# Kernel optimization log

Measured on AMD Instinct MI355X. Metric: run time of the kernel, lower is better.

## Reference

```python
import jax, jax.numpy as jnp
import numpy as np

GROUPS = 32
EPS = 1e-5


def _group_norm(x, w, b):
    B, C, H, W = x.shape
    xr = x.reshape(B, GROUPS, C // GROUPS, H, W)
    mean = xr.mean(axis=(2, 3, 4), keepdims=True)
    var = xr.var(axis=(2, 3, 4), keepdims=True)
    xn = ((xr - mean) * jax.lax.rsqrt(var + EPS)).reshape(B, C, H, W)
    return xn * w[None, :, None, None] + b[None, :, None, None]


def _conv1x1(w, b, x):
    # 1x1 conv == per-pixel channel matmul
    return jnp.einsum('oc,bchw->bohw', w, x) + b[None, :, None, None]


def setup_inputs() -> dict:
    key = jax.random.key(0)
    ks = jax.random.split(key, 6)
    C = 512
    s = 1.0 / np.sqrt(C)  # kaiming-uniform-ish scale for 1x1 convs
    return {
        'x': jax.random.normal(ks[0], (4, C, 64, 64), jnp.float32),
        'gn_w': jnp.ones((C,), jnp.float32),
        'gn_b': jnp.zeros((C,), jnp.float32),
        'qw': jax.random.normal(ks[1], (C, C), jnp.float32) * s,
        'qb': jnp.zeros((C,), jnp.float32),
        'kw': jax.random.normal(ks[2], (C, C), jnp.float32) * s,
        'kb': jnp.zeros((C,), jnp.float32),
        'vw': jax.random.normal(ks[3], (C, C), jnp.float32) * s,
        'vb': jnp.zeros((C,), jnp.float32),
        'pw': jax.random.normal(ks[4], (C, C), jnp.float32) * s,
        'pb': jnp.zeros((C,), jnp.float32),
    }


def reference(x, gn_w, gn_b, qw, qb, kw, kb, vw, vb, pw, pb):
    B, C, H, W = x.shape
    h_ = _group_norm(x, gn_w, gn_b)
    q = _conv1x1(qw, qb, h_).reshape(B, C, H * W)
    k = _conv1x1(kw, kb, h_).reshape(B, C, H * W)
    v = _conv1x1(vw, vb, h_).reshape(B, C, H * W)
    # scores [B, HW(query), HW(key)]
    scores = jnp.einsum('bcq,bck->bqk', q, k) * (C ** -0.5)
    attn = jax.nn.softmax(scores, axis=-1)
    out = jnp.einsum('bqk,bdk->bdq', attn, v).reshape(B, C, H, W)
    return x + _conv1x1(pw, pb, out)
```

## Files before the change

### kernel.cpp

```cpp
#include <hip/hip_runtime.h>

#define DEV __device__ __forceinline__

typedef __attribute__((ext_vector_type(8))) short short8;
typedef __attribute__((ext_vector_type(4))) float floatx4;
typedef __attribute__((ext_vector_type(16))) float floatx16;
typedef __attribute__((ext_vector_type(4))) int i32x4;
typedef __attribute__((ext_vector_type(8))) int i32x8;

DEV unsigned short f2bs(float x) {
    unsigned u = __float_as_uint(x);
    unsigned r = (u + 0x7fffu + ((u >> 16) & 1u)) >> 16;
    return (unsigned short)r;
}

DEV unsigned char f2fp8(float x) {
#if __has_builtin(__builtin_amdgcn_cvt_pk_fp8_f32)
    int pk = __builtin_amdgcn_cvt_pk_fp8_f32(x, 0.f, 0, false);
    return (unsigned char)(pk & 0xff);
#else
    unsigned u = __float_as_uint(x);
    unsigned s = (u >> 24) & 0x80;
    unsigned a = u & 0x7fffffff;
    unsigned um = a + 0x7ffffu + ((a >> 20) & 1u);
    unsigned r = (a >= 0x3c800000u) ? ((um >> 20) - 0x3C0u) : 0u;
    return (unsigned char)(r | s);
#endif
}

DEV unsigned pack_fp8x4(float v0, float v1, float v2, float v3) {
#if __has_builtin(__builtin_amdgcn_cvt_pk_fp8_f32)
    unsigned pk = (unsigned)__builtin_amdgcn_cvt_pk_fp8_f32(v0, v1, 0, false);
    pk = (unsigned)__builtin_amdgcn_cvt_pk_fp8_f32(v2, v3, (int)pk, true);
    return pk;
#else
    return (unsigned)f2fp8(v0) | ((unsigned)f2fp8(v1) << 8) |
           ((unsigned)f2fp8(v2) << 16) | ((unsigned)f2fp8(v3) << 24);
#endif
}

DEV unsigned pack_i8x4(float v0, float v1, float v2, float v3) {
    unsigned b0 = (unsigned)((int)rintf(v0)) & 255u;
    unsigned b1 = (unsigned)((int)rintf(v1)) & 255u;
    unsigned b2 = (unsigned)((int)rintf(v2)) & 255u;
    unsigned b3 = (unsigned)((int)rintf(v3)) & 255u;
    return b0 | (b1 << 8) | (b2 << 16) | (b3 << 24);
}

DEV void syncfull() {
    asm volatile("s_waitcnt vmcnt(0) lgkmcnt(0)" ::: "memory");
    __builtin_amdgcn_sched_barrier(0);
    __builtin_amdgcn_s_barrier();
    __builtin_amdgcn_sched_barrier(0);
}

__global__ void pre_kernel(const float* __restrict__ x,
                           const float* __restrict__ qw, const float* __restrict__ kw,
                           const float* __restrict__ vw, const float* __restrict__ pw,
                           const float* __restrict__ qb, const float* __restrict__ kb,
                           unsigned short* __restrict__ wqkb, unsigned short* __restrict__ wvb,
                           unsigned short* __restrict__ wpb,
                           float* __restrict__ biasqk,
                           float* __restrict__ stats) {
    int b = blockIdx.x, tid = threadIdx.x;
    if (b < 768) {
        const float* src = (b < 256) ? qw : (b < 512) ? kw : vw;
        unsigned short* dst = (b < 256) ? wqkb : (b < 512) ? (wqkb + 262144) : wvb;
        int off = (b & 255) * 256 + tid;
        float4 v = ((const float4*)src)[off];
        ushort4 o;
        o.x = f2bs(v.x); o.y = f2bs(v.y); o.z = f2bs(v.z); o.w = f2bs(v.w);
        ((ushort4*)dst)[off] = o;
    } else if (b < 1024) {
        int off = (b - 768) * 256 + tid;
        int row = off >> 7, c4 = (off & 127) * 4;
        float4 v = ((const float4*)pw)[off];
        float vv[4] = {v.x, v.y, v.z, v.w};
#pragma unroll
        for (int e = 0; e < 4; ++e) {
            int c = c4 + e;
            int cp = (c & ~63) | (((c & 31) << 1) | ((c >> 5) & 1));
            wpb[row * 512 + cp] = f2bs(vv[e]);
        }
    } else if (b == 1024) {
        biasqk[tid]       = qb[tid];
        biasqk[256 + tid] = qb[256 + tid];
        biasqk[512 + tid] = kb[tid];
        biasqk[768 + tid] = kb[256 + tid];
    } else {
        int bg = b - 1025;
        const float4* p = (const float4*)(x + (size_t)bg * 65536);
        float s = 0.f, ss = 0.f;
        for (int i = tid; i < 16384; i += 256) {
            float4 v = p[i];
            s += v.x + v.y + v.z + v.w;
            ss += v.x * v.x + v.y * v.y + v.z * v.z + v.w * v.w;
        }
        for (int off = 32; off; off >>= 1) { s += __shfl_down(s, off); ss += __shfl_down(ss, off); }
        __shared__ float rs[4], rss[4];
        int wave = tid >> 6, lane = tid & 63;
        if (lane == 0) { rs[wave] = s; rss[wave] = ss; }
        __syncthreads();
        if (tid == 0) {
            float S = rs[0] + rs[1] + rs[2] + rs[3];
            float SS = rss[0] + rss[1] + rss[2] + rss[3];
            float mean = S * (1.f / 65536.f);
            float var = SS * (1.f / 65536.f) - mean * mean;
            stats[bg * 2] = mean;
            stats[bg * 2 + 1] = rsqrtf(var + 1e-5f);
        }
    }
}

__global__ void gn_apply_kernel(const float* __restrict__ x, const float* __restrict__ stats,
                                const float* __restrict__ gw, const float* __restrict__ gb,
                                unsigned short* __restrict__ ht) {
    __shared__ __align__(16) unsigned short t[64][72];
    int b = blockIdx.z, c0 = blockIdx.y * 64, p0 = blockIdx.x * 64;
    int tid = threadIdx.x;
    const float* xb = x + ((size_t)b * 512 + c0) * 4096 + p0;
#pragma unroll
    for (int pass = 0; pass < 4; ++pass) {
        int cl = pass * 16 + (tid >> 4);
        int pq = (tid & 15) * 4;
        float4 v = *(const float4*)(xb + (size_t)cl * 4096 + pq);
        int c = c0 + cl, g = c >> 4;
        float mean = stats[(b * 32 + g) * 2], rstd = stats[(b * 32 + g) * 2 + 1];
        float sw = gw[c] * rstd;
        float sb = gb[c] - mean * sw;
        t[pq + 0][cl] = f2bs(v.x * sw + sb);
        t[pq + 1][cl] = f2bs(v.y * sw + sb);
        t[pq + 2][cl] = f2bs(v.z * sw + sb);
        t[pq + 3][cl] = f2bs(v.w * sw + sb);
    }
    __syncthreads();
    unsigned short* hb = ht + ((size_t)b * 4096 + p0) * 512 + c0;
#pragma unroll
    for (int pass = 0; pass < 2; ++pass) {
        int pl = pass * 32 + (tid >> 3);
        int c8 = (tid & 7) * 8;
        *(uint4*)(hb + (size_t)pl * 512 + c8) = *(const uint4*)&t[pl][c8];
    }
}

__global__ void gemm_qkv(const unsigned short* __restrict__ h_t, long long sP,
                         const unsigned short* __restrict__ wqkb,
                         const unsigned short* __restrict__ wvb,
                         char* __restrict__ q_i8, char* __restrict__ k_i8,
                         char* __restrict__ v_f8,
                         const float* __restrict__ biasqk, const float* __restrict__ vb,
                         float qs) {
    __shared__ __align__(16) unsigned short lA[128 * 64];
    __shared__ __align__(16) unsigned short lB[128 * 64];
    const int tid = threadIdx.x;
    const int wave = tid >> 6, lane = tid & 63;
    const int flat = blockIdx.x;
    const bool isqk = flat < 1024;
    int m0, n0, bz;
    const unsigned short *Ab, *Bb;
    if (isqk) {
        m0 = ((flat >> 3) & 31) * 128;
        n0 = (flat & 7) * 128;
        bz = flat >> 8;
        Ab = h_t + (size_t)bz * sP;
        Bb = wqkb;
    } else {
        const int g = flat - 1024;
        m0 = ((g >> 5) & 3) * 128;
        n0 = (g & 31) * 128;
        bz = g >> 7;
        Ab = wvb;
        Bb = h_t + (size_t)bz * sP;
    }

    floatx4 acc[4][4];
#pragma unroll
    for (int i = 0; i < 4; i++)
#pragma unroll
        for (int j = 0; j < 4; j++) acc[i][j] = (floatx4){0.f, 0.f, 0.f, 0.f};

    const int wm = (wave >> 1) * 64, wn = (wave & 1) * 64;
    const int quad = lane >> 4;
    const int lc = lane & 15;
    const int lc7 = lc & 7;

    for (int kt = 0; kt < 8; ++kt) {
        const int kbase = kt * 64;
#pragma unroll
        for (int c = 0; c < 4; ++c) {
            int d = c * 256 + tid;
            int r = d >> 3;
            int kc = (d & 7) ^ (r & 7);
            const unsigned short* ga = Ab + (size_t)(m0 + r) * 512 + kbase + kc * 8;
            const unsigned short* gb = Bb + (size_t)(n0 + r) * 512 + kbase + kc * 8;
            __builtin_amdgcn_global_load_lds(
                (const __attribute__((address_space(1))) void*)ga,
                (__attribute__((address_space(3))) void*)&lA[(size_t)(c * 256 + wave * 64) * 8], 16, 0, 0);
            __builtin_amdgcn_global_load_lds(
                (const __attribute__((address_space(1))) void*)gb,
                (__attribute__((address_space(3))) void*)&lB[(size_t)(c * 256 + wave * 64) * 8], 16, 0, 0);
        }
        __syncthreads();
#pragma unroll
        for (int kk = 0; kk < 2; ++kk) {
            const int swz = ((kk * 4 + quad) ^ lc7) * 8;
            short8 af[4], bf[4];
#pragma unroll
            for (int i = 0; i < 4; i++)
                af[i] = *(const short8*)&lA[(size_t)(wm + i * 16 + lc) * 64 + swz];
#pragma unroll
            for (int j = 0; j < 4; j++)
                bf[j] = *(const short8*)&lB[(size_t)(wn + j * 16 + lc) * 64 + swz];
#pragma unroll
            for (int i = 0; i < 4; i++)
#pragma unroll
                for (int j = 0; j < 4; j++)
                    acc[i][j] = __builtin_amdgcn_mfma_f32_16x16x32_bf16(af[i], bf[j], acc[i][j], 0, 0, 0);
        }
        __syncthreads();
    }

    const int rowb = quad * 4;
    if (isqk) {
#pragma unroll
        for (int i = 0; i < 4; i++) {
#pragma unroll
            for (int r = 0; r < 4; r++) {
                const int m = m0 + wm + i * 16 + rowb + r;
                float q[4];
#pragma unroll
                for (int j = 0; j < 4; j++) {
                    const int n = n0 + wn + j * 16 + lc;
                    q[j] = fminf(fmaxf((acc[i][j][r] + biasqk[n]) * qs, -127.f), 127.f);
                }
                const int col64 = n0 + wn;
                char* outp = (col64 < 512) ? q_i8 : k_i8;
                size_t idx = (size_t)bz * sP + (size_t)m * 512 +
                             (col64 - ((col64 < 512) ? 0 : 512)) + lc * 4;
                *(unsigned*)(outp + idx) = pack_i8x4(q[0], q[1], q[2], q[3]);
            }
        }
    } else {
#pragma unroll
        for (int i = 0; i < 4; i++) {
#pragma unroll
            for (int r = 0; r < 4; r++) {
                const int m = m0 + wm + i * 16 + rowb + r;
                const float bm = vb[m];
                float q[4];
#pragma unroll
                for (int j = 0; j < 4; j++)
                    q[j] = fminf(fmaxf(acc[i][j][r] + bm, -448.f), 448.f);
                size_t idx = (size_t)bz * sP + (size_t)m * 4096 + n0 + wn + lc * 4;
                *(unsigned*)(v_f8 + idx) = pack_fp8x4(q[0], q[1], q[2], q[3]);
            }
        }
    }
}

__global__ void gemm_proj(const unsigned short* __restrict__ A,
                          const unsigned short* __restrict__ B, long long sBb,
                          float* __restrict__ Cv, long long sCb,
                          const float* __restrict__ bias,
                          const float* __restrict__ resid, long long sRb,
                          const float* __restrict__ rsum,
                          int M, int N, int K) {
    __shared__ __align__(16) unsigned short lA[128 * 64];
    __shared__ __align__(16) unsigned short lB[128 * 64];
    const int tid = threadIdx.x;
    const int wave = tid >> 6, lane = tid & 63;
    const int m0 = blockIdx.y * 128, n0 = blockIdx.x * 128, bz = blockIdx.z;
    const unsigned short* Ab = A;
    const unsigned short* Bb = B + (size_t)bz * sBb;

    floatx4 acc[4][4];
#pragma unroll
    for (int i = 0; i < 4; i++)
#pragma unroll
        for (int j = 0; j < 4; j++) acc[i][j] = (floatx4){0.f, 0.f, 0.f, 0.f};

    const int wm = (wave >> 1) * 64, wn = (wave & 1) * 64;
    const int quad = lane >> 4;
    const int lc = lane & 15;
    const int lc7 = lc & 7;

    const int nk = K >> 6;
    for (int kt = 0; kt < nk; ++kt) {
        const int kbase = kt * 64;
#pragma unroll
        for (int c = 0; c < 4; ++c) {
            int d = c * 256 + tid;
            int r = d >> 3;
            int kc = (d & 7) ^ (r & 7);
            const unsigned short* ga = Ab + (size_t)(m0 + r) * 512 + ((kbase & 511) + kc * 8);
            const unsigned short* gb = Bb + (size_t)(n0 + r) * 1024 + kbase + kc * 8;
            __builtin_amdgcn_global_load_lds(
                (const __attribute__((address_space(1))) void*)ga,
                (__attribute__((address_space(3))) void*)&lA[(size_t)(c * 256 + wave * 64) * 8], 16, 0, 0);
            __builtin_amdgcn_global_load_lds(
                (const __attribute__((address_space(1))) void*)gb,
                (__attribute__((address_space(3))) void*)&lB[(size_t)(c * 256 + wave * 64) * 8], 16, 0, 0);
        }
        __syncthreads();
#pragma unroll
        for (int kk = 0; kk < 2; ++kk) {
            const int swz = ((kk * 4 + quad) ^ lc7) * 8;
            short8 af[4], bf[4];
#pragma unroll
            for (int i = 0; i < 4; i++)
                af[i] = *(const short8*)&lA[(size_t)(wm + i * 16 + lc) * 64 + swz];
#pragma unroll
            for (int j = 0; j < 4; j++)
                bf[j] = *(const short8*)&lB[(size_t)(wn + j * 16 + lc) * 64 + swz];
#pragma unroll
            for (int i = 0; i < 4; i++)
#pragma unroll
                for (int j = 0; j < 4; j++)
                    acc[i][j] = __builtin_amdgcn_mfma_f32_16x16x32_bf16(af[i], bf[j], acc[i][j], 0, 0, 0);
        }
        __syncthreads();
    }

    float rsinv[4];
#pragma unroll
    for (int j = 0; j < 4; j++) {
        const int n = n0 + wn + j * 16 + lc;
        rsinv[j] = 1.f / (rsum[(size_t)bz * 4096 + n] + rsum[(size_t)(4 + bz) * 4096 + n]);
    }

    const int rowb = quad * 4;
#pragma unroll
    for (int i = 0; i < 4; i++) {
#pragma unroll
        for (int r = 0; r < 4; r++) {
            const int m = m0 + wm + i * 16 + rowb + r;
            const float bm = bias[m];
#pragma unroll
            for (int j = 0; j < 4; j++) {
                const int n = n0 + wn + j * 16 + lc;
                size_t idx = (size_t)bz * sCb + (size_t)m * N + n;
                Cv[idx] = acc[i][j][r] * rsinv[j] + bm + resid[(size_t)bz * sRb + (size_t)m * N + n];
            }
        }
    }
}

__global__ __launch_bounds__(512, 2) void attn_fused(
    const char* __restrict__ Qg, const char* __restrict__ Kg,
    const char* __restrict__ Vg,
    unsigned short* __restrict__ Ou, long long sOb,
    float* __restrict__ rsum, float scale2) {
    __shared__ __align__(16) char Kl[256 * 128];
    __shared__ __align__(16) char Vl[256 * 128];
    __shared__ __align__(16) char Pl[64 * 128];
    const int tid = threadIdx.x;
    const int wave = tid >> 6, lane = tid & 63;
    const int quad = lane >> 4, lc = lane & 15;
    const int lc7 = lc & 7;
    const int l31 = lane & 31, lh = lane >> 5;
    const int id = blockIdx.x;
    const int xcd = id & 7, qi = id >> 3;
    const int bz = xcd >> 1, split = xcd & 1;
    const int q0 = qi * 128;
    const int kvbase = split * 2048;
    const int NIT = 32;

    const char* Kb = Kg + ((size_t)bz * 4096 + kvbase) * 512;
    const char* Vb = Vg + (size_t)bz * 2097152 + kvbase;

    const int wq = wave * 16;
    const int mO = (wave >> 2) * 64, nO = (wave & 3) * 128;
    const int q = wq + lc;

    i32x4 qreg[8];
    {
        const char* Qrow = Qg + ((size_t)bz * 4096 + q0 + q) * 512 + quad * 16;
#pragma unroll
        for (int ks = 0; ks < 8; ++ks)
            qreg[ks] = *(const i32x4*)(Qrow + ks * 64);
    }

    auto stageK = [&](int t) {
#pragma unroll
        for (int c = 0; c < 4; ++c) {
            int f = c * 512 + tid;
            int rr = f >> 3, cs = f & 7;
            int kv = rr & 63, chq = rr >> 6;
            int s = cs ^ (kv & 7);
            __builtin_amdgcn_global_load_lds(
                (const __attribute__((address_space(1))) void*)(Kb + (size_t)(t * 64 + kv) * 512 + chq * 128 + s * 16),
                (__attribute__((address_space(3))) void*)(Kl + (size_t)f * 16), 16, 0, 0);
        }
    };
    auto stageV = [&](int t) {
#pragma unroll
        for (int c = 0; c < 4; ++c) {
            int f = c * 512 + tid;
            int u = (f & 7) ^ ((f >> 3) & 7);
            int d = ((f >> 3) << 1) | (u >> 2);
            int gq = u & 3;
            __builtin_amdgcn_global_load_lds(
                (const __attribute__((address_space(1))) void*)(Vb + (size_t)d * 4096 + t * 64 + gq * 16),
                (__attribute__((address_space(3))) void*)(Vl + (size_t)f * 16), 16, 0, 0);
        }
    };

    floatx16 acco[2][4];
#pragma unroll
    for (int i = 0; i < 2; ++i)
#pragma unroll
        for (int j = 0; j < 4; ++j)
#pragma unroll
            for (int r = 0; r < 16; ++r) acco[i][j][r] = 0.f;
    float rs = 0.f;

    stageK(0);
    stageV(0);
    syncfull();

    for (int t = 0; t < NIT; ++t) {
        if (t > 0) stageV(t);
        i32x4 accs[4];
#pragma unroll
        for (int ki = 0; ki < 4; ++ki) accs[ki] = (i32x4){0, 0, 0, 0};
        __builtin_amdgcn_s_setprio(1);
#pragma unroll
        for (int ks = 0; ks < 8; ++ks) {
            const int g = ks * 4 + quad;
            const int gh = g >> 3, gl = g & 7;
#pragma unroll
            for (int ki = 0; ki < 4; ++ki) {
                const int ar = ki * 16 + lc;
                i32x4 afrag = *(const i32x4*)&Kl[(size_t)(gh * 64 + ar) * 128 + ((gl ^ (ar & 7)) << 4)];
                accs[ki] = __builtin_amdgcn_mfma_i32_16x16x64_i8(afrag, qreg[ks], accs[ki], 0, 0, 0);
            }
        }
        __builtin_amdgcn_s_setprio(0);
        float e[4][4];
#pragma unroll
        for (int ki = 0; ki < 4; ++ki)
#pragma unroll
            for (int r = 0; r < 4; ++r) {
                e[ki][r] = fminf(exp2f(fmaf((float)accs[ki][r], scale2, -2.0f)), 448.f);
                rs += e[ki][r];
            }
        {
            unsigned w0 = pack_fp8x4(e[0][0], e[1][0], e[2][0], e[3][0]);
            unsigned w1 = pack_fp8x4(e[0][1], e[1][1], e[2][1], e[3][1]);
            unsigned w2 = pack_fp8x4(e[0][2], e[1][2], e[2][2], e[3][2]);
            unsigned w3 = pack_fp8x4(e[0][3], e[1][3], e[2][3], e[3][3]);
            const int L = q >> 1;
            const int sl = ((((q & 1) << 2) | quad) ^ (L & 7));
            *(i32x4*)&Pl[(size_t)L * 128 + (sl << 4)] = (i32x4){(int)w0, (int)w1, (int)w2, (int)w3};
        }
        syncfull();

        if (t + 1 < NIT) stageK(t + 1);
        {
            i32x8 pa[2], vv[4];
#pragma unroll
            for (int i = 0; i < 2; ++i) {
                const int r_ = mO + i * 32 + l31;
                const int L = r_ >> 1;
                const int sb = ((r_ & 1) << 2) | (lh << 1);
                i32x4 lo = *(const i32x4*)&Pl[(size_t)L * 128 + ((sb ^ (L & 7)) << 4)];
                i32x4 hi = *(const i32x4*)&Pl[(size_t)L * 128 + (((sb | 1) ^ (L & 7)) << 4)];
                pa[i] = __builtin_shufflevector(lo, hi, 0, 1, 2, 3, 4, 5, 6, 7);
            }
#pragma unroll
            for (int j = 0; j < 4; ++j) {
                const int r_ = nO + j * 32 + l31;
                const int L = r_ >> 1;
                const int sb = ((r_ & 1) << 2) | (lh << 1);
                i32x4 lo = *(const i32x4*)&Vl[(size_t)L * 128 + ((sb ^ (L & 7)) << 4)];
                i32x4 hi = *(const i32x4*)&Vl[(size_t)L * 128 + (((sb | 1) ^ (L & 7)) << 4)];
                vv[j] = __builtin_shufflevector(lo, hi, 0, 1, 2, 3, 4, 5, 6, 7);
            }
#pragma unroll
            for (int i = 0; i < 2; ++i)
#pragma unroll
                for (int j = 0; j < 4; ++j)
                    acco[i][j] = __builtin_amdgcn_mfma_scale_f32_32x32x64_f8f6f4(
                        pa[i], vv[j], acco[i][j], 0, 0,
                        0, 0x7f7f7f7f, 0, 0x7f7f7f7f);
        }
        syncfull();
    }

    rs += __shfl_xor(rs, 16);
    rs += __shfl_xor(rs, 32);
    if (quad == 0) rsum[((size_t)(split * 4 + bz)) * 4096 + q0 + q] = rs;

#pragma unroll
    for (int i = 0; i < 2; ++i) {
#pragma unroll
        for (int reg = 0; reg < 16; ++reg) {
            const int m = q0 + mO + i * 32 + (reg & 3) + 8 * (reg >> 2) + 4 * lh;
            unsigned u01 = (unsigned)f2bs(acco[i][0][reg]) | ((unsigned)f2bs(acco[i][1][reg]) << 16);
            unsigned u23 = (unsigned)f2bs(acco[i][2][reg]) | ((unsigned)f2bs(acco[i][3][reg]) << 16);
            unsigned short* base = Ou + (size_t)bz * sOb + (size_t)m * 1024 + split * 512 + nO;
            *(unsigned*)(base + l31 * 2) = u01;
            *(unsigned*)(base + 64 + l31 * 2) = u23;
        }
    }
}

extern "C" void kernel_launch(void* const* d_in, const int* in_sizes, int n_in,
                              void* d_out, int out_size, void* d_ws, size_t ws_size,
                              hipStream_t stream) {
    (void)in_sizes; (void)n_in; (void)out_size; (void)ws_size;
    const float* x   = (const float*)d_in[0];
    const float* gnw = (const float*)d_in[1];
    const float* gnb = (const float*)d_in[2];
    const float* qw  = (const float*)d_in[3];
    const float* qb  = (const float*)d_in[4];
    const float* kw  = (const float*)d_in[5];
    const float* kb  = (const float*)d_in[6];
    const float* vw  = (const float*)d_in[7];
    const float* vb  = (const float*)d_in[8];
    const float* pw  = (const float*)d_in[9];
    const float* pb  = (const float*)d_in[10];
    float* out = (float*)d_out;

    char* ws = (char*)d_ws;
    unsigned short* h_t = (unsigned short*)(ws);
    char* q_i8 = (char*)(ws + (16ull << 20));
    char* k_i8 = (char*)(ws + (32ull << 20));
    char* v_f8 = (char*)(ws + (48ull << 20));
    unsigned short* wqkb = (unsigned short*)(ws + (64ull << 20));
    unsigned short* wvb = (unsigned short*)(ws + (65ull << 20));
    unsigned short* wpb = wvb + 262144;
    float* stats  = (float*)(ws + (66ull << 20));
    float* biasqk = (float*)(ws + (66ull << 20) + 8192);
    float* rowsum = (float*)(ws + (66ull << 20) + 65536);
    unsigned short* o_un = (unsigned short*)(ws + (72ull << 20));

    const long long sP  = 2097152;
    const long long sOb = 4194304;
    const float QS = 16.f;
    const float SC = 0.044194173824159216f / (QS * QS);
    const float LOG2E = 1.4426950408889634f;

    pre_kernel<<<1153, 256, 0, stream>>>(x, qw, kw, vw, pw, qb, kb, wqkb, wvb, wpb,
                                         biasqk, stats);
    gn_apply_kernel<<<dim3(64, 8, 4), 256, 0, stream>>>(x, stats, gnw, gnb, h_t);
    gemm_qkv<<<1536, 256, 0, stream>>>(h_t, sP, wqkb, wvb, q_i8, k_i8, v_f8, biasqk, vb, QS);
    attn_fused<<<dim3(256), 512, 0, stream>>>(q_i8, k_i8, v_f8, o_un, sOb, rowsum,
                                              SC * LOG2E);
    gemm_proj<<<dim3(32, 4, 4), 256, 0, stream>>>(wpb, o_un, sOb, out, sP, pb, x, sP,
                                                  rowsum, 512, 4096, 1024);
}
```

Baseline: 284.9 us.

## Process two KV tiles per attention iteration to halve block barriers

The fused attention loop now stages two 64-key K and V tiles into separate LDS buffers and computes QK, exp and P for both before one barrier. It then runs PV for both tiles. This halves the number of block-wide synchronisations per KV sweep and keeps more global-to-LDS loads in flight. The cost is LDS use growing to about 144KB per block, which allows at most one resident block per CU, plus higher register pressure from the larger unrolled body.

```diff
diff --git a/kernel.cpp b/kernel.cpp
--- a/kernel.cpp
+++ b/kernel.cpp
@@ -350,20 +350,19 @@
     const char* __restrict__ Vg,
     unsigned short* __restrict__ Ou, long long sOb,
     float* __restrict__ rsum, float scale2) {
-    __shared__ __align__(16) char Kl[256 * 128];
-    __shared__ __align__(16) char Vl[256 * 128];
-    __shared__ __align__(16) char Pl[64 * 128];
+    __shared__ __align__(16) char Kl[2][256 * 128];
+    __shared__ __align__(16) char Vl[2][256 * 128];
+    __shared__ __align__(16) char Pl[2][64 * 128];
     const int tid = threadIdx.x;
     const int wave = tid >> 6, lane = tid & 63;
     const int quad = lane >> 4, lc = lane & 15;
-    const int lc7 = lc & 7;
     const int l31 = lane & 31, lh = lane >> 5;
     const int id = blockIdx.x;
     const int xcd = id & 7, qi = id >> 3;
     const int bz = xcd >> 1, split = xcd & 1;
     const int q0 = qi * 128;
     const int kvbase = split * 2048;
-    const int NIT = 32;
+    const int NP = 16;
 
     const char* Kb = Kg + ((size_t)bz * 4096 + kvbase) * 512;
     const char* Vb = Vg + (size_t)bz * 2097152 + kvbase;
@@ -380,19 +379,19 @@
             qreg[ks] = *(const i32x4*)(Qrow + ks * 64);
     }
 
-    auto stageK = [&](int t) {
+    auto stageK = [&](int s, int t) {
 #pragma unroll
         for (int c = 0; c < 4; ++c) {
             int f = c * 512 + tid;
             int rr = f >> 3, cs = f & 7;
             int kv = rr & 63, chq = rr >> 6;
-            int s = cs ^ (kv & 7);
+            int sl = cs ^ (kv & 7);
             __builtin_amdgcn_global_load_lds(
-                (const __attribute__((address_space(1))) void*)(Kb + (size_t)(t * 64 + kv) * 512 + chq * 128 + s * 16),
-                (__attribute__((address_space(3))) void*)(Kl + (size_t)f * 16), 16, 0, 0);
+                (const __attribute__((address_space(1))) void*)(Kb + (size_t)(t * 64 + kv) * 512 + chq * 128 + sl * 16),
+                (__attribute__((address_space(3))) void*)(Kl[s] + (size_t)f * 16), 16, 0, 0);
         }
     };
-    auto stageV = [&](int t) {
+    auto stageV = [&](int s, int t) {
 #pragma unroll
         for (int c = 0; c < 4; ++c) {
             int f = c * 512 + tid;
@@ -401,7 +400,7 @@
             int gq = u & 3;
             __builtin_amdgcn_global_load_lds(
                 (const __attribute__((address_space(1))) void*)(Vb + (size_t)d * 4096 + t * 64 + gq * 16),
-                (__attribute__((address_space(3))) void*)(Vl + (size_t)f * 16), 16, 0, 0);
+                (__attribute__((address_space(3))) void*)(Vl[s] + (size_t)f * 16), 16, 0, 0);
         }
     };
 
@@ -414,12 +413,7 @@
             for (int r = 0; r < 16; ++r) acco[i][j][r] = 0.f;
     float rs = 0.f;
 
-    stageK(0);
-    stageV(0);
-    syncfull();
-
-    for (int t = 0; t < NIT; ++t) {
-        if (t > 0) stageV(t);
+    auto qk_sub = [&](int s) {
         i32x4 accs[4];
 #pragma unroll
         for (int ki = 0; ki < 4; ++ki) accs[ki] = (i32x4){0, 0, 0, 0};
@@ -431,7 +425,7 @@
 #pragma unroll
             for (int ki = 0; ki < 4; ++ki) {
                 const int ar = ki * 16 + lc;
-                i32x4 afrag = *(const i32x4*)&Kl[(size_t)(gh * 64 + ar) * 128 + ((gl ^ (ar & 7)) << 4)];
+                i32x4 afrag = *(const i32x4*)&Kl[s][(size_t)(gh * 64 + ar) * 128 + ((gl ^ (ar & 7)) << 4)];
                 accs[ki] = __builtin_amdgcn_mfma_i32_16x16x64_i8(afrag, qreg[ks], accs[ki], 0, 0, 0);
             }
         }
@@ -444,27 +438,36 @@
                 e[ki][r] = fminf(exp2f(fmaf((float)accs[ki][r], scale2, -2.0f)), 448.f);
                 rs += e[ki][r];
             }
-        {
-            unsigned w0 = pack_fp8x4(e[0][0], e[1][0], e[2][0], e[3][0]);
-            unsigned w1 = pack_fp8x4(e[0][1], e[1][1], e[2][1], e[3][1]);
-            unsigned w2 = pack_fp8x4(e[0][2], e[1][2], e[2][2], e[3][2]);
-            unsigned w3 = pack_fp8x4(e[0][3], e[1][3], e[2][3], e[3][3]);
-            const int L = q >> 1;
-            const int sl = ((((q & 1) << 2) | quad) ^ (L & 7));
-            *(i32x4*)&Pl[(size_t)L * 128 + (sl << 4)] = (i32x4){(int)w0, (int)w1, (int)w2, (int)w3};
-        }
+        unsigned w0 = pack_fp8x4(e[0][0], e[1][0], e[2][0], e[3][0]);
+        unsigned w1 = pack_fp8x4(e[0][1], e[1][1], e[2][1], e[3][1]);
+        unsigned w2 = pack_fp8x4(e[0][2], e[1][2], e[2][2], e[3][2]);
+        unsigned w3 = pack_fp8x4(e[0][3], e[1][3], e[2][3], e[3][3]);
+        const int L = q >> 1;
+        const int sl = ((((q & 1) << 2) | quad) ^ (L & 7));
+        *(i32x4*)&Pl[s][(size_t)L * 128 + (sl << 4)] = (i32x4){(int)w0, (int)w1, (int)w2, (int)w3};
+    };
+
+    stageK(0, 0); stageK(1, 1);
+    stageV(0, 0); stageV(1, 1);
+    syncfull();
+
+    for (int T = 0; T < NP; ++T) {
+        if (T > 0) { stageV(0, 2 * T); stageV(1, 2 * T + 1); }
+        qk_sub(0);
+        qk_sub(1);
         syncfull();
-
-        if (t + 1 < NIT) stageK(t + 1);
-        {
+        if (T + 1 < NP) { stageK(0, 2 * T + 2); stageK(1, 2 * T + 3); }
+
+#pragma unroll
+        for (int s = 0; s < 2; ++s) {
             i32x8 pa[2], vv[4];
 #pragma unroll
             for (int i = 0; i < 2; ++i) {
                 const int r_ = mO + i * 32 + l31;
                 const int L = r_ >> 1;
                 const int sb = ((r_ & 1) << 2) | (lh << 1);
-                i32x4 lo = *(const i32x4*)&Pl[(size_t)L * 128 + ((sb ^ (L & 7)) << 4)];
-                i32x4 hi = *(const i32x4*)&Pl[(size_t)L * 128 + (((sb | 1) ^ (L & 7)) << 4)];
+                i32x4 lo = *(const i32x4*)&Pl[s][(size_t)L * 128 + ((sb ^ (L & 7)) << 4)];
+                i32x4 hi = *(const i32x4*)&Pl[s][(size_t)L * 128 + (((sb | 1) ^ (L & 7)) << 4)];
                 pa[i] = __builtin_shufflevector(lo, hi, 0, 1, 2, 3, 4, 5, 6, 7);
             }
 #pragma unroll
@@ -472,8 +475,8 @@
                 const int r_ = nO + j * 32 + l31;
                 const int L = r_ >> 1;
                 const int sb = ((r_ & 1) << 2) | (lh << 1);
-                i32x4 lo = *(const i32x4*)&Vl[(size_t)L * 128 + ((sb ^ (L & 7)) << 4)];
-                i32x4 hi = *(const i32x4*)&Vl[(size_t)L * 128 + (((sb | 1) ^ (L & 7)) << 4)];
+                i32x4 lo = *(const i32x4*)&Vl[s][(size_t)L * 128 + ((sb ^ (L & 7)) << 4)];
+                i32x4 hi = *(const i32x4*)&Vl[s][(size_t)L * 128 + (((sb | 1) ^ (L & 7)) << 4)];
                 vv[j] = __builtin_shufflevector(lo, hi, 0, 1, 2, 3, 4, 5, 6, 7);
             }
 #pragma unroll
```

Result: no change. 287.9 us (+1.0%).

## Specialize waves: half compute QK scores, half stage K/V loads

Applied to the files above, without the earlier changes.

Splits the eight waves of the fused attention block into two roles. Waves 0-3 each compute scores for 32 query rows, reusing each K fragment across two query groups. Waves 4-7 issue all the K/V global-to-LDS staging loads. This cuts the K fragment LDS reads per MFMA and keeps the DMA issue off the score-computing waves. In exchange, half the waves sit idle during the QK phase and the score waves hold twice as many Q registers.

```diff
diff --git a/kernel.cpp b/kernel.cpp
--- a/kernel.cpp
+++ b/kernel.cpp
@@ -356,7 +356,6 @@
     const int tid = threadIdx.x;
     const int wave = tid >> 6, lane = tid & 63;
     const int quad = lane >> 4, lc = lane & 15;
-    const int lc7 = lc & 7;
     const int l31 = lane & 31, lh = lane >> 5;
     const int id = blockIdx.x;
     const int xcd = id & 7, qi = id >> 3;
@@ -364,26 +363,29 @@
     const int q0 = qi * 128;
     const int kvbase = split * 2048;
     const int NIT = 32;
+    const bool qkw = (wave < 4);
+    const int stid = tid & 255;
 
     const char* Kb = Kg + ((size_t)bz * 4096 + kvbase) * 512;
     const char* Vb = Vg + (size_t)bz * 2097152 + kvbase;
 
-    const int wq = wave * 16;
     const int mO = (wave >> 2) * 64, nO = (wave & 3) * 128;
-    const int q = wq + lc;
-
-    i32x4 qreg[8];
-    {
-        const char* Qrow = Qg + ((size_t)bz * 4096 + q0 + q) * 512 + quad * 16;
-#pragma unroll
-        for (int ks = 0; ks < 8; ++ks)
-            qreg[ks] = *(const i32x4*)(Qrow + ks * 64);
+
+    i32x4 qreg[2][8];
+    if (qkw) {
+#pragma unroll
+        for (int g = 0; g < 2; ++g) {
+            const char* Qrow = Qg + ((size_t)bz * 4096 + q0 + wave * 32 + g * 16 + lc) * 512 + quad * 16;
+#pragma unroll
+            for (int ks = 0; ks < 8; ++ks)
+                qreg[g][ks] = *(const i32x4*)(Qrow + ks * 64);
+        }
     }
 
     auto stageK = [&](int t) {
 #pragma unroll
-        for (int c = 0; c < 4; ++c) {
-            int f = c * 512 + tid;
+        for (int c = 0; c < 8; ++c) {
+            int f = c * 256 + stid;
             int rr = f >> 3, cs = f & 7;
             int kv = rr & 63, chq = rr >> 6;
             int s = cs ^ (kv & 7);
@@ -394,8 +396,8 @@
     };
     auto stageV = [&](int t) {
 #pragma unroll
-        for (int c = 0; c < 4; ++c) {
-            int f = c * 512 + tid;
+        for (int c = 0; c < 8; ++c) {
+            int f = c * 256 + stid;
             int u = (f & 7) ^ ((f >> 3) & 7);
             int d = ((f >> 3) << 1) | (u >> 2);
             int gq = u & 3;
@@ -412,50 +414,61 @@
         for (int j = 0; j < 4; ++j)
 #pragma unroll
             for (int r = 0; r < 16; ++r) acco[i][j][r] = 0.f;
-    float rs = 0.f;
-
-    stageK(0);
-    stageV(0);
+    float rsv[2] = {0.f, 0.f};
+
+    if (!qkw) { stageK(0); stageV(0); }
     syncfull();
 
     for (int t = 0; t < NIT; ++t) {
-        if (t > 0) stageV(t);
-        i32x4 accs[4];
-#pragma unroll
-        for (int ki = 0; ki < 4; ++ki) accs[ki] = (i32x4){0, 0, 0, 0};
-        __builtin_amdgcn_s_setprio(1);
-#pragma unroll
-        for (int ks = 0; ks < 8; ++ks) {
-            const int g = ks * 4 + quad;
-            const int gh = g >> 3, gl = g & 7;
-#pragma unroll
-            for (int ki = 0; ki < 4; ++ki) {
-                const int ar = ki * 16 + lc;
-                i32x4 afrag = *(const i32x4*)&Kl[(size_t)(gh * 64 + ar) * 128 + ((gl ^ (ar & 7)) << 4)];
-                accs[ki] = __builtin_amdgcn_mfma_i32_16x16x64_i8(afrag, qreg[ks], accs[ki], 0, 0, 0);
-            }
-        }
-        __builtin_amdgcn_s_setprio(0);
-        float e[4][4];
-#pragma unroll
-        for (int ki = 0; ki < 4; ++ki)
-#pragma unroll
-            for (int r = 0; r < 4; ++r) {
-                e[ki][r] = fminf(exp2f(fmaf((float)accs[ki][r], scale2, -2.0f)), 448.f);
-                rs += e[ki][r];
-            }
-        {
-            unsigned w0 = pack_fp8x4(e[0][0], e[1][0], e[2][0], e[3][0]);
-            unsigned w1 = pack_fp8x4(e[0][1], e[1][1], e[2][1], e[3][1]);
-            unsigned w2 = pack_fp8x4(e[0][2], e[1][2], e[2][2], e[3][2]);
-            unsigned w3 = pack_fp8x4(e[0][3], e[1][3], e[2][3], e[3][3]);
-            const int L = q >> 1;
-            const int sl = ((((q & 1) << 2) | quad) ^ (L & 7));
-            *(i32x4*)&Pl[(size_t)L * 128 + (sl << 4)] = (i32x4){(int)w0, (int)w1, (int)w2, (int)w3};
+        if (qkw) {
+            i32x4 accs[2][4];
+#pragma unroll
+            for (int g = 0; g < 2; ++g)
+#pragma unroll
+                for (int ki = 0; ki < 4; ++ki) accs[g][ki] = (i32x4){0, 0, 0, 0};
+            __builtin_amdgcn_s_setprio(1);
+#pragma unroll
+            for (int ks = 0; ks < 8; ++ks) {
+                const int g4 = ks * 4 + quad;
+                const int gh = g4 >> 3, gl = g4 & 7;
+                i32x4 afrag[4];
+#pragma unroll
+                for (int ki = 0; ki < 4; ++ki) {
+                    const int ar = ki * 16 + lc;
+                    afrag[ki] = *(const i32x4*)&Kl[(size_t)(gh * 64 + ar) * 128 + ((gl ^ (ar & 7)) << 4)];
+                }
+#pragma unroll
+                for (int g = 0; g < 2; ++g)
+#pragma unroll
+                    for (int ki = 0; ki < 4; ++ki)
+                        accs[g][ki] = __builtin_amdgcn_mfma_i32_16x16x64_i8(afrag[ki], qreg[g][ks], accs[g][ki], 0, 0, 0);
+            }
+            __builtin_amdgcn_s_setprio(0);
+#pragma unroll
+            for (int g = 0; g < 2; ++g) {
+                float e[4][4];
+#pragma unroll
+                for (int ki = 0; ki < 4; ++ki)
+#pragma unroll
+                    for (int r = 0; r < 4; ++r) {
+                        e[ki][r] = fminf(exp2f(fmaf((float)accs[g][ki][r], scale2, -2.0f)), 448.f);
+                        rsv[g] += e[ki][r];
+                    }
+                unsigned w0 = pack_fp8x4(e[0][0], e[1][0], e[2][0], e[3][0]);
+                unsigned w1 = pack_fp8x4(e[0][1], e[1][1], e[2][1], e[3][1]);
+                unsigned w2 = pack_fp8x4(e[0][2], e[1][2], e[2][2], e[3][2]);
+                unsigned w3 = pack_fp8x4(e[0][3], e[1][3], e[2][3], e[3][3]);
+                const int row = wave * 32 + g * 16 + lc;
+                const int L = row >> 1;
+                const int sl = ((((row & 1) << 2) | quad) ^ (L & 7));
+                *(i32x4*)&Pl[(size_t)L * 128 + (sl << 4)] = (i32x4){(int)w0, (int)w1, (int)w2, (int)w3};
+            }
+        } else {
+            if (t > 0) stageV(t);
         }
         syncfull();
 
-        if (t + 1 < NIT) stageK(t + 1);
+        if (!qkw && t + 1 < NIT) stageK(t + 1);
         {
             i32x8 pa[2], vv[4];
 #pragma unroll
@@ -487,9 +500,16 @@
         syncfull();
     }
 
-    rs += __shfl_xor(rs, 16);
-    rs += __shfl_xor(rs, 32);
-    if (quad == 0) rsum[((size_t)(split * 4 + bz)) * 4096 + q0 + q] = rs;
+    if (qkw) {
+#pragma unroll
+        for (int g = 0; g < 2; ++g) {
+            float rs = rsv[g];
+            rs += __shfl_xor(rs, 16);
+            rs += __shfl_xor(rs, 32);
+            if (quad == 0)
+                rsum[((size_t)(split * 4 + bz)) * 4096 + q0 + wave * 32 + g * 16 + lc] = rs;
+        }
+    }
 
 #pragma unroll
     for (int i = 0; i < 2; ++i) {
```

New measurement: 332.2 us. 1.17x slower.
